# Optimization experiments

Measured on AMD Instinct MI355X. Metric: run time of the kernel, lower is better.

The kernel has to match this reference:

```python
import jax, jax.numpy as jnp
import numpy as np

INITIAL_RADIUS = 1.0


def setup_inputs() -> dict:
    key = jax.random.key(0)
    k1, k2, k3 = jax.random.split(key, 3)
    B, N, S = 4, 8192, 2048
    xyz = jax.random.normal(k1, (B, 3, N), dtype=jnp.float32)
    sparse_xyz = jax.random.normal(k2, (B, 3, S), dtype=jnp.float32)
    sparse_flow = jax.random.normal(k3, (B, 3, S), dtype=jnp.float32)
    return {"xyz": xyz, "sparse_xyz": sparse_xyz, "sparse_flow": sparse_flow,
            "resol_factor": 1}


def reference(xyz, sparse_xyz, sparse_flow, resol_factor):
    # xyz: [B,3,N], sparse_xyz/sparse_flow: [B,3,S]
    radius = INITIAL_RADIUS * resol_factor
    x = jnp.transpose(xyz, (0, 2, 1))          # [B,N,3] dense query points
    y = jnp.transpose(sparse_xyz, (0, 2, 1))   # [B,S,3] sparse support points
    f = jnp.transpose(sparse_flow, (0, 2, 1))  # [B,S,3] sparse flow values
    B, S, _ = y.shape
    w = jnp.ones((B, S, 1), dtype=x.dtype)     # uniform sample weights

    # squared pairwise distances D2[b,n,s] = ||x_bn - y_bs||^2
    x2 = jnp.sum(x * x, axis=-1, keepdims=True)            # [B,N,1]
    y2 = jnp.sum(y * y, axis=-1)[:, None, :]               # [B,1,S]
    xy = jnp.einsum('bnd,bsd->bns', x, y)                  # [B,N,S]
    d2 = x2 + y2 - 2.0 * xy

    # Gaussian Nadaraya-Watson kernel weights
    k = jnp.exp(-d2 / (radius * radius))                   # [B,N,S]

    num = jnp.einsum('bns,bsd->bnd', k, f * w)             # [B,N,3]
    den = jnp.einsum('bns,bsd->bnd', k, w)                 # [B,N,1]
    dense = num / den                                      # [B,N,3]
    return jnp.transpose(dense, (0, 2, 1))                 # [B,3,N]
```

## Files before the change

### kernel.cpp

```cpp
#include <hip/hip_runtime.h>


constexpr int B_ = 4, N_ = 8192, S_ = 2048;
constexpr int BLOCK = 256, PPT = 4;
constexpr int PTS_PER_BLOCK = BLOCK * PPT;
constexpr int NB = (B_ * N_) / PTS_PER_BLOCK;
constexpr int BN = B_ * N_;
constexpr float LOG2E = 1.4426950408889634f;

template <int CHUNK>
__global__ __launch_bounds__(BLOCK, 2) void uf2_partial(
    const float* __restrict__ xyz,
    const float* __restrict__ sxyz,
    const float* __restrict__ sflow,
    const int* __restrict__ resol,
    float4* __restrict__ part)
{
    __shared__ float4 As[CHUNK];
    __shared__ float4 Fs[CHUNK];

    const int nb = blockIdx.x % NB;
    const int sc = blockIdx.x / NB;
    const int b  = nb >> 3;
    const int n0 = (nb & 7) * PTS_PER_BLOCK;
    const int s0 = sc * CHUNK;

    const float r      = (float)resol[0];
    const float inv_r2 = 1.0f / (r * r);
    const float c2 = 2.0f * inv_r2 * LOG2E;
    const float cy = -inv_r2 * LOG2E;

    const float* ybase = sxyz  + b * 3 * S_;
    const float* fbase = sflow + b * 3 * S_;
    for (int t = threadIdx.x; t < CHUNK; t += BLOCK) {
        const int s = s0 + t;
        const float yx = ybase[s], yy = ybase[S_ + s], yz = ybase[2 * S_ + s];
        const float fx = fbase[s], fy = fbase[S_ + s], fz = fbase[2 * S_ + s];
        As[t] = make_float4(yx, yy, yz, cy * (yx * yx + yy * yy + yz * yz));
        Fs[t] = make_float4(fx, fy, fz, 0.0f);
    }
    __syncthreads();

    const float* xbase = xyz + b * 3 * N_;
    float px[PPT], py[PPT], pz[PPT];
    float4 acc[PPT];
#pragma unroll
    for (int p = 0; p < PPT; ++p) {
        const int n = n0 + threadIdx.x + p * BLOCK;
        px[p] = xbase[n];
        py[p] = xbase[N_ + n];
        pz[p] = xbase[2 * N_ + n];
        acc[p] = make_float4(0.f, 0.f, 0.f, 0.f);
    }

#pragma unroll 4
    for (int t = 0; t < CHUNK; ++t) {
        const float4 a = As[t];
        const float4 f = Fs[t];
#pragma unroll
        for (int p = 0; p < PPT; ++p) {
            float dot = px[p] * a.x;
            dot = fmaf(py[p], a.y, dot);
            dot = fmaf(pz[p], a.z, dot);
            const float k = __builtin_amdgcn_exp2f(fmaf(dot, c2, a.w));
            acc[p].x = fmaf(k, f.x, acc[p].x);
            acc[p].y = fmaf(k, f.y, acc[p].y);
            acc[p].z = fmaf(k, f.z, acc[p].z);
            acc[p].w += k;
        }
    }

#pragma unroll
    for (int p = 0; p < PPT; ++p) {
        const int g = b * N_ + n0 + threadIdx.x + p * BLOCK;
        part[(size_t)sc * BN + g] = acc[p];
    }
}

__global__ __launch_bounds__(256) void uf2_combine(
    const float4* __restrict__ part, float* __restrict__ out, int SC)
{
    const int g = blockIdx.x * 256 + threadIdx.x;
    float4 s = make_float4(0.f, 0.f, 0.f, 0.f);
    for (int c = 0; c < SC; ++c) {
        const float4 p = part[(size_t)c * BN + g];
        s.x += p.x; s.y += p.y; s.z += p.z; s.w += p.w;
    }
    const float inv = 1.0f / s.w;
    const int b = g >> 13;
    const int n = g & (N_ - 1);
    float* ob = out + b * 3 * N_;
    ob[n]          = s.x * inv;
    ob[N_ + n]     = s.y * inv;
    ob[2 * N_ + n] = s.z * inv;
}

__global__ __launch_bounds__(BLOCK, 1) void uf2_fused(
    const float* __restrict__ xyz,
    const float* __restrict__ sxyz,
    const float* __restrict__ sflow,
    const int* __restrict__ resol,
    float* __restrict__ out)
{
    __shared__ float4 As[S_];
    __shared__ float4 Fs[S_];

    const int nb = blockIdx.x;
    const int b  = nb >> 3;
    const int n0 = (nb & 7) * PTS_PER_BLOCK;

    const float r      = (float)resol[0];
    const float inv_r2 = 1.0f / (r * r);
    const float c2 = 2.0f * inv_r2 * LOG2E;
    const float cy = -inv_r2 * LOG2E;

    const float* ybase = sxyz  + b * 3 * S_;
    const float* fbase = sflow + b * 3 * S_;
    for (int t = threadIdx.x; t < S_; t += BLOCK) {
        const float yx = ybase[t], yy = ybase[S_ + t], yz = ybase[2 * S_ + t];
        const float fx = fbase[t], fy = fbase[S_ + t], fz = fbase[2 * S_ + t];
        As[t] = make_float4(yx, yy, yz, cy * (yx * yx + yy * yy + yz * yz));
        Fs[t] = make_float4(fx, fy, fz, 0.0f);
    }
    __syncthreads();

    const float* xbase = xyz + b * 3 * N_;
    float px[PPT], py[PPT], pz[PPT];
    float4 acc[PPT];
#pragma unroll
    for (int p = 0; p < PPT; ++p) {
        const int n = n0 + threadIdx.x + p * BLOCK;
        px[p] = xbase[n];
        py[p] = xbase[N_ + n];
        pz[p] = xbase[2 * N_ + n];
        acc[p] = make_float4(0.f, 0.f, 0.f, 0.f);
    }

#pragma unroll 4
    for (int t = 0; t < S_; ++t) {
        const float4 a = As[t];
        const float4 f = Fs[t];
#pragma unroll
        for (int p = 0; p < PPT; ++p) {
            float dot = px[p] * a.x;
            dot = fmaf(py[p], a.y, dot);
            dot = fmaf(pz[p], a.z, dot);
            const float k = __builtin_amdgcn_exp2f(fmaf(dot, c2, a.w));
            acc[p].x = fmaf(k, f.x, acc[p].x);
            acc[p].y = fmaf(k, f.y, acc[p].y);
            acc[p].z = fmaf(k, f.z, acc[p].z);
            acc[p].w += k;
        }
    }

#pragma unroll
    for (int p = 0; p < PPT; ++p) {
        const int n = n0 + threadIdx.x + p * BLOCK;
        const float inv = 1.0f / acc[p].w;
        float* ob = out + b * 3 * N_;
        ob[n]          = acc[p].x * inv;
        ob[N_ + n]     = acc[p].y * inv;
        ob[2 * N_ + n] = acc[p].z * inv;
    }
}

extern "C" void kernel_launch(void* const* d_in, const int* in_sizes, int n_in,
                              void* d_out, int out_size, void* d_ws, size_t ws_size,
                              hipStream_t stream)
{
    const float* xyz   = (const float*)d_in[0];
    const float* sxyz  = (const float*)d_in[1];
    const float* sflow = (const float*)d_in[2];
    const int*   resol = (const int*)d_in[3];
    float* out   = (float*)d_out;
    float4* part = (float4*)d_ws;

    const size_t per_chunk = (size_t)BN * sizeof(float4);
    int SC = 16;
    while (SC > 1 && (size_t)SC * per_chunk > ws_size) SC >>= 1;

    if ((size_t)SC * per_chunk > ws_size) {
        uf2_fused<<<dim3(NB), dim3(BLOCK), 0, stream>>>(xyz, sxyz, sflow, resol, out);
        return;
    }

    dim3 grid(NB * SC), blk(BLOCK);
    switch (SC) {
        case 16: uf2_partial<S_ / 16><<<grid, blk, 0, stream>>>(xyz, sxyz, sflow, resol, part); break;
        case 8:  uf2_partial<S_ / 8 ><<<grid, blk, 0, stream>>>(xyz, sxyz, sflow, resol, part); break;
        case 4:  uf2_partial<S_ / 4 ><<<grid, blk, 0, stream>>>(xyz, sxyz, sflow, resol, part); break;
        case 2:  uf2_partial<S_ / 2 ><<<grid, blk, 0, stream>>>(xyz, sxyz, sflow, resol, part); break;
        default: uf2_partial<S_     ><<<grid, blk, 0, stream>>>(xyz, sxyz, sflow, resol, part); break;
    }
    uf2_combine<<<dim3(BN / 256), dim3(256), 0, stream>>>(part, out, SC);
}
```

Measured before the change: 32.06 us.

## Precompute per-support exp factor and read support data from global memory

Adds a prep kernel that factors exp(-|y|^2/r^2) into the flow and weight terms and prescales y by 2/r^2, so each inner iteration needs only a 3-term dot product and one exp2. The main kernel drops shared-memory staging and reads 32-byte support records straight from global memory, where every lane loads the same address. Each thread now handles one query point instead of four. This removes one fma per pair and the LDS staging, but it costs an extra launch, adds an 8-float global load per support point that is no longer amortized over four points, and risks overflow or underflow, since exp of the squared norm and exp of the dot product are now computed separately.

```diff
diff --git a/kernel.cpp b/kernel.cpp
--- a/kernel.cpp
+++ b/kernel.cpp
@@ -1,86 +1,75 @@
 #include <hip/hip_runtime.h>
 
 
+typedef __attribute__((ext_vector_type(8))) float f8;
+
 constexpr int B_ = 4, N_ = 8192, S_ = 2048;
-constexpr int BLOCK = 256, PPT = 4;
-constexpr int PTS_PER_BLOCK = BLOCK * PPT;
-constexpr int NB = (B_ * N_) / PTS_PER_BLOCK;
+constexpr int BLOCK = 256;
+constexpr int NBPB = N_ / BLOCK;
+constexpr int NB = B_ * NBPB;
 constexpr int BN = B_ * N_;
 constexpr float LOG2E = 1.4426950408889634f;
 
-template <int CHUNK>
-__global__ __launch_bounds__(BLOCK, 2) void uf2_partial(
-    const float* __restrict__ xyz,
+__global__ __launch_bounds__(BLOCK) void uf2_prep(
     const float* __restrict__ sxyz,
     const float* __restrict__ sflow,
     const int* __restrict__ resol,
-    float4* __restrict__ part)
+    f8* __restrict__ P)
 {
-    __shared__ float4 As[CHUNK];
-    __shared__ float4 Fs[CHUNK];
-
-    const int nb = blockIdx.x % NB;
-    const int sc = blockIdx.x / NB;
-    const int b  = nb >> 3;
-    const int n0 = (nb & 7) * PTS_PER_BLOCK;
-    const int s0 = sc * CHUNK;
-
-    const float r      = (float)resol[0];
+    const int i = blockIdx.x * BLOCK + threadIdx.x;
+    const int b = i / S_;
+    const int s = i - b * S_;
+    const float r = (float)resol[0];
     const float inv_r2 = 1.0f / (r * r);
     const float c2 = 2.0f * inv_r2 * LOG2E;
     const float cy = -inv_r2 * LOG2E;
+    const float* yb = sxyz  + b * 3 * S_;
+    const float* fb = sflow + b * 3 * S_;
+    const float yx = yb[s], yy = yb[S_ + s], yz = yb[2 * S_ + s];
+    const float fx = fb[s], fy = fb[S_ + s], fz = fb[2 * S_ + s];
+    const float ky = __builtin_amdgcn_exp2f(cy * (yx * yx + yy * yy + yz * yz));
+    f8 v;
+    v[0] = c2 * yx; v[1] = c2 * yy; v[2] = c2 * yz; v[3] = 0.0f;
+    v[4] = ky * fx; v[5] = ky * fy; v[6] = ky * fz; v[7] = ky;
+    P[i] = v;
+}
 
-    const float* ybase = sxyz  + b * 3 * S_;
-    const float* fbase = sflow + b * 3 * S_;
-    for (int t = threadIdx.x; t < CHUNK; t += BLOCK) {
-        const int s = s0 + t;
-        const float yx = ybase[s], yy = ybase[S_ + s], yz = ybase[2 * S_ + s];
-        const float fx = fbase[s], fy = fbase[S_ + s], fz = fbase[2 * S_ + s];
-        As[t] = make_float4(yx, yy, yz, cy * (yx * yx + yy * yy + yz * yz));
-        Fs[t] = make_float4(fx, fy, fz, 0.0f);
-    }
-    __syncthreads();
+template <int CHUNK>
+__global__ __launch_bounds__(BLOCK) void uf2_main(
+    const float* __restrict__ xyz,
+    const f8* __restrict__ P,
+    float4* __restrict__ part)
+{
+    const int nb = blockIdx.x % NB;
+    const int sc = blockIdx.x / NB;
+    const int b  = nb / NBPB;
+    const int n  = (nb % NBPB) * BLOCK + threadIdx.x;
 
-    const float* xbase = xyz + b * 3 * N_;
-    float px[PPT], py[PPT], pz[PPT];
-    float4 acc[PPT];
-#pragma unroll
-    for (int p = 0; p < PPT; ++p) {
-        const int n = n0 + threadIdx.x + p * BLOCK;
-        px[p] = xbase[n];
-        py[p] = xbase[N_ + n];
-        pz[p] = xbase[2 * N_ + n];
-        acc[p] = make_float4(0.f, 0.f, 0.f, 0.f);
+    const float* xb = xyz + b * 3 * N_;
+    const float px = xb[n], py = xb[N_ + n], pz = xb[2 * N_ + n];
+
+    const f8* __restrict__ p = P + b * S_ + sc * CHUNK;
+
+    float ax = 0.f, ay = 0.f, az = 0.f, aw = 0.f;
+#pragma unroll 8
+    for (int t = 0; t < CHUNK; ++t) {
+        const f8 v = p[t];
+        float e = fmaf(px, v[0], fmaf(py, v[1], pz * v[2]));
+        const float k = __builtin_amdgcn_exp2f(e);
+        ax = fmaf(k, v[4], ax);
+        ay = fmaf(k, v[5], ay);
+        az = fmaf(k, v[6], az);
+        aw = fmaf(k, v[7], aw);
     }
 
-#pragma unroll 4
-    for (int t = 0; t < CHUNK; ++t) {
-        const float4 a = As[t];
-        const float4 f = Fs[t];
-#pragma unroll
-        for (int p = 0; p < PPT; ++p) {
-            float dot = px[p] * a.x;
-            dot = fmaf(py[p], a.y, dot);
-            dot = fmaf(pz[p], a.z, dot);
-            const float k = __builtin_amdgcn_exp2f(fmaf(dot, c2, a.w));
-            acc[p].x = fmaf(k, f.x, acc[p].x);
-            acc[p].y = fmaf(k, f.y, acc[p].y);
-            acc[p].z = fmaf(k, f.z, acc[p].z);
-            acc[p].w += k;
-        }
-    }
-
-#pragma unroll
-    for (int p = 0; p < PPT; ++p) {
-        const int g = b * N_ + n0 + threadIdx.x + p * BLOCK;
-        part[(size_t)sc * BN + g] = acc[p];
-    }
+    const int g = b * N_ + n;
+    part[(size_t)sc * BN + g] = make_float4(ax, ay, az, aw);
 }
 
-__global__ __launch_bounds__(256) void uf2_combine(
+__global__ __launch_bounds__(BLOCK) void uf2_combine(
     const float4* __restrict__ part, float* __restrict__ out, int SC)
 {
-    const int g = blockIdx.x * 256 + threadIdx.x;
+    const int g = blockIdx.x * BLOCK + threadIdx.x;
     float4 s = make_float4(0.f, 0.f, 0.f, 0.f);
     for (int c = 0; c < SC; ++c) {
         const float4 p = part[(size_t)c * BN + g];
@@ -102,40 +91,39 @@
     const int* __restrict__ resol,
     float* __restrict__ out)
 {
+    constexpr int PPT = 4;
+    constexpr int PTS = BLOCK * PPT;
     __shared__ float4 As[S_];
     __shared__ float4 Fs[S_];
 
     const int nb = blockIdx.x;
-    const int b  = nb >> 3;
-    const int n0 = (nb & 7) * PTS_PER_BLOCK;
+    const int b  = nb / (N_ / PTS);
+    const int n0 = (nb % (N_ / PTS)) * PTS;
 
-    const float r      = (float)resol[0];
+    const float r = (float)resol[0];
     const float inv_r2 = 1.0f / (r * r);
     const float c2 = 2.0f * inv_r2 * LOG2E;
     const float cy = -inv_r2 * LOG2E;
 
-    const float* ybase = sxyz  + b * 3 * S_;
-    const float* fbase = sflow + b * 3 * S_;
+    const float* yb = sxyz  + b * 3 * S_;
+    const float* fb = sflow + b * 3 * S_;
     for (int t = threadIdx.x; t < S_; t += BLOCK) {
-        const float yx = ybase[t], yy = ybase[S_ + t], yz = ybase[2 * S_ + t];
-        const float fx = fbase[t], fy = fbase[S_ + t], fz = fbase[2 * S_ + t];
+        const float yx = yb[t], yy = yb[S_ + t], yz = yb[2 * S_ + t];
+        const float fx = fb[t], fy = fb[S_ + t], fz = fb[2 * S_ + t];
         As[t] = make_float4(yx, yy, yz, cy * (yx * yx + yy * yy + yz * yz));
         Fs[t] = make_float4(fx, fy, fz, 0.0f);
     }
     __syncthreads();
 
-    const float* xbase = xyz + b * 3 * N_;
+    const float* xb = xyz + b * 3 * N_;
     float px[PPT], py[PPT], pz[PPT];
     float4 acc[PPT];
 #pragma unroll
     for (int p = 0; p < PPT; ++p) {
         const int n = n0 + threadIdx.x + p * BLOCK;
-        px[p] = xbase[n];
-        py[p] = xbase[N_ + n];
-        pz[p] = xbase[2 * N_ + n];
+        px[p] = xb[n]; py[p] = xb[N_ + n]; pz[p] = xb[2 * N_ + n];
         acc[p] = make_float4(0.f, 0.f, 0.f, 0.f);
     }
-
 #pragma unroll 4
     for (int t = 0; t < S_; ++t) {
         const float4 a = As[t];
@@ -152,7 +140,6 @@
             acc[p].w += k;
         }
     }
-
 #pragma unroll
     for (int p = 0; p < PPT; ++p) {
         const int n = n0 + threadIdx.x + p * BLOCK;
@@ -172,25 +159,32 @@
     const float* sxyz  = (const float*)d_in[1];
     const float* sflow = (const float*)d_in[2];
     const int*   resol = (const int*)d_in[3];
-    float* out   = (float*)d_out;
-    float4* part = (float4*)d_ws;
+    float* out = (float*)d_out;
 
+    const size_t P_bytes = (size_t)1 << 20;
     const size_t per_chunk = (size_t)BN * sizeof(float4);
     int SC = 16;
-    while (SC > 1 && (size_t)SC * per_chunk > ws_size) SC >>= 1;
+    while (SC > 1 && P_bytes + (size_t)SC * per_chunk > ws_size) SC >>= 1;
 
-    if ((size_t)SC * per_chunk > ws_size) {
-        uf2_fused<<<dim3(NB), dim3(BLOCK), 0, stream>>>(xyz, sxyz, sflow, resol, out);
+    if (P_bytes + (size_t)SC * per_chunk > ws_size) {
+        uf2_fused<<<dim3(BN / 1024), dim3(BLOCK), 0, stream>>>(
+            xyz, sxyz, sflow, resol, out);
         return;
     }
 
+    f8* P = (f8*)d_ws;
+    float4* part = (float4*)((char*)d_ws + P_bytes);
+
+    uf2_prep<<<dim3((B_ * S_) / BLOCK), dim3(BLOCK), 0, stream>>>(
+        sxyz, sflow, resol, P);
+
     dim3 grid(NB * SC), blk(BLOCK);
     switch (SC) {
-        case 16: uf2_partial<S_ / 16><<<grid, blk, 0, stream>>>(xyz, sxyz, sflow, resol, part); break;
-        case 8:  uf2_partial<S_ / 8 ><<<grid, blk, 0, stream>>>(xyz, sxyz, sflow, resol, part); break;
-        case 4:  uf2_partial<S_ / 4 ><<<grid, blk, 0, stream>>>(xyz, sxyz, sflow, resol, part); break;
-        case 2:  uf2_partial<S_ / 2 ><<<grid, blk, 0, stream>>>(xyz, sxyz, sflow, resol, part); break;
-        default: uf2_partial<S_     ><<<grid, blk, 0, stream>>>(xyz, sxyz, sflow, resol, part); break;
+        case 16: uf2_main<S_ / 16><<<grid, blk, 0, stream>>>(xyz, P, part); break;
+        case 8:  uf2_main<S_ / 8 ><<<grid, blk, 0, stream>>>(xyz, P, part); break;
+        case 4:  uf2_main<S_ / 4 ><<<grid, blk, 0, stream>>>(xyz, P, part); break;
+        case 2:  uf2_main<S_ / 2 ><<<grid, blk, 0, stream>>>(xyz, P, part); break;
+        default: uf2_main<S_     ><<<grid, blk, 0, stream>>>(xyz, P, part); break;
     }
-    uf2_combine<<<dim3(BN / 256), dim3(256), 0, stream>>>(part, out, SC);
+    uf2_combine<<<dim3(BN / BLOCK), dim3(BLOCK), 0, stream>>>(part, out, SC);
 }
```

New measurement: 32.58 us. About the same (+1.6%).
